# Kernel tuning notes

Hardware: AMD Instinct MI355X
Metric: run time of the kernel (lower is better)

Reference implementation:

```python
import jax, jax.numpy as jnp
import numpy as np

C = 0.01          # curvature
SQRT_C = C ** 0.5 # 0.1
R = 16            # number of diagonal blocks = out_features / block_size
BS = 256          # block_size
D = R * BS        # 4096


def _artanh(x):
    # Matches torch Artanh: clamp input, grad is 1/(1-xc^2) (straight-through clamp)
    xc = jnp.clip(x, -1.0 + 1e-5, 1.0 - 1e-5)
    xc = x + jax.lax.stop_gradient(xc - x)
    return 0.5 * (jnp.log(1.0 + xc) - jnp.log(1.0 - xc))


def _tanh(x, clamp=15.0):
    return jnp.tanh(jnp.clip(x, -clamp, clamp))


def _norm(x):
    return jnp.linalg.norm(x, axis=-1, keepdims=True)


def _forward(x, weights):
    # expmap0 (poincare ball)
    u_norm = jnp.maximum(_norm(x), 1e-5)
    h = _tanh(SQRT_C * u_norm) * x / (SQRT_C * u_norm)
    # fix_filt = output_hyperbolic.data  -> detach
    h = jax.lax.stop_gradient(h)

    # mobius_matvec with block-diagonal weight; equivalent batched block matmul:
    # mx = h @ block_diag(W_1..W_r).T  ==  per-block h_r @ W_r.T
    xb = h.reshape(h.shape[:-1] + (R, BS))            # [..., r, bs]
    mx = jnp.einsum('...rk,rjk->...rj', xb, weights)  # [..., r, bs]
    mx = mx.reshape(h.shape)

    x_norm = jnp.maximum(_norm(h), 1e-5)
    mx_norm = _norm(mx)
    res_c = _tanh(mx_norm / x_norm * _artanh(SQRT_C * x_norm)) * mx / (mx_norm * SQRT_C)
    cond = jnp.all(mx == 0, axis=-1, keepdims=True)
    res = jnp.where(cond, jnp.zeros((), dtype=res_c.dtype), res_c)

    # _project onto the ball
    nrm = jnp.maximum(_norm(res), 1e-5)
    maxnorm = (1.0 - 1e-3) / SQRT_C
    res = jnp.where(nrm > maxnorm, res / nrm * maxnorm, res)

    # logmap0 (poincare ball)
    y_norm = jnp.maximum(_norm(res), 1e-5)
    return res / y_norm / SQRT_C * _artanh(SQRT_C * y_norm)


def setup_inputs() -> dict:
    key = jax.random.key(0)
    k1, k2 = jax.random.split(key)
    x = jax.random.normal(k1, (4, 2048, D), dtype=jnp.float32)
    # params: init is stack of identity blocks; add small noise so math is non-trivial
    eye = jnp.broadcast_to(jnp.eye(BS, dtype=jnp.float32), (R, BS, BS))
    weights = eye + 0.02 * jax.random.normal(k2, (R, BS, BS), dtype=jnp.float32)
    return {"x": x, "weights": weights}


def reference(x, weights):
    return _forward(x, weights)
```

## Files before the change

kernel.cpp:

```cpp
#include <hip/hip_runtime.h>
#include <hip/hip_fp16.h>


typedef __attribute__((ext_vector_type(8))) short short8;
typedef __attribute__((ext_vector_type(4))) float f32x4;
typedef __attribute__((ext_vector_type(16))) float f32x16;

__device__ __forceinline__ ushort f2bf(float f) {
  uint u = __float_as_uint(f);
  return (ushort)((u + 0x7fffu + ((u >> 16) & 1u)) >> 16);
}

__device__ __forceinline__ float gamma_of(float sx, float s2) {
  const float xnorm = sqrtf(sx);
  const float un = fmaxf(xnorm, 1e-5f);
  const float a0 = 0.1f * un;
  const float th = tanhf(fminf(a0, 15.f));
  const float c = th / a0;
  const float hn = th * (xnorm / a0);
  const float xn = fmaxf(hn, 1e-5f);
  const float sp = sqrtf(s2);
  float gt = 0.f;
  if (sp > 0.f) {
    const float s = c * sp;
    const float xc = fminf(0.1f * xn, 1.f - 1e-5f);
    const float at = 0.5f * logf((1.f + xc) / (1.f - xc));
    const float t = (s / xn) * at;
    const float tn = tanhf(fminf(t, 15.f));
    const float alpha = tn / (0.1f * s);
    const float rn = tn * 10.f;
    const float nrm = fmaxf(rn, 1e-5f);
    const float proj = (nrm > 9.99f) ? (9.99f / nrm) : 1.f;
    const float yn = fmaxf(rn * proj, 1e-5f);
    const float yc = fminf(0.1f * yn, 1.f - 1e-5f);
    const float at2 = 0.5f * logf((1.f + yc) / (1.f - yc));
    gt = c * alpha * proj * (at2 / (0.1f * yn));
  }
  return gt;
}

__global__ __launch_bounds__(256) void wrepack32(const float* __restrict__ w,
                                                 ushort* __restrict__ wb3) {
  int idx = blockIdx.x * 256 + threadIdx.x;
  int lane = idx & 63;
  int nt = (idx >> 6) & 7;
  int kf = (idx >> 9) & 15;
  int b = idx >> 13;
  int n = nt * 32 + (lane & 31);
  int k0 = kf * 16 + (lane >> 5) * 8;
  const float* src = w + ((size_t)b << 16) + (size_t)n * 256 + k0;
  float4 v0 = *reinterpret_cast<const float4*>(src);
  float4 v1 = *reinterpret_cast<const float4*>(src + 4);
  uint4 p;
  p.x = (uint)f2bf(v0.x) | ((uint)f2bf(v0.y) << 16);
  p.y = (uint)f2bf(v0.z) | ((uint)f2bf(v0.w) << 16);
  p.z = (uint)f2bf(v1.x) | ((uint)f2bf(v1.y) << 16);
  p.w = (uint)f2bf(v1.z) | ((uint)f2bf(v1.w) << 16);
  reinterpret_cast<uint4*>(wb3)[idx] = p;
}

__global__ __launch_bounds__(256, 2) void k1_kernel(const float* __restrict__ x,
                                                    const ushort* __restrict__ wb3,
                                                    float* __restrict__ ssxP,
                                                    float* __restrict__ sspP,
                                                    ushort* __restrict__ mxw) {
  const int tid = threadIdx.x;
  const int w = tid >> 6;
  const int l = tid & 63;
  const int lo = l & 31;
  const int hi = l >> 5;
  const int b = blockIdx.x & 15;
  const int rg = blockIdx.x >> 4;
  const ushort* bbase = wb3 + ((size_t)b << 16);

  short8 B0[16], B1[16];
#pragma unroll
  for (int kf = 0; kf < 16; ++kf) {
    B0[kf] = *reinterpret_cast<const short8*>(bbase + (size_t)(kf * 8 + w * 2 + 0) * 512 + l * 8);
    B1[kf] = *reinterpret_cast<const short8*>(bbase + (size_t)(kf * 8 + w * 2 + 1) * 512 + l * 8);
  }

  for (int t = 0; t < 8; ++t) {
    const int rt = rg * 8 + t;
    const float* abase = x + ((size_t)rt * 32 + lo) * 4096 + b * 256 + hi * 8;

    f32x16 a0, a1;
#pragma unroll
    for (int r = 0; r < 16; ++r) { a0[r] = 0.f; a1[r] = 0.f; }
    float ssl = 0.f;

#pragma unroll
    for (int bb4 = 0; bb4 < 4; ++bb4) {
      float4 va[8];
#pragma unroll
      for (int k4 = 0; k4 < 4; ++k4) {
        const int kf = bb4 * 4 + k4;
        va[k4 * 2 + 0] = *reinterpret_cast<const float4*>(abase + kf * 16);
        va[k4 * 2 + 1] = *reinterpret_cast<const float4*>(abase + kf * 16 + 4);
      }
      if (w == 0) {
#pragma unroll
        for (int i = 0; i < 8; ++i)
          ssl += va[i].x * va[i].x + va[i].y * va[i].y + va[i].z * va[i].z + va[i].w * va[i].w;
      }
#pragma unroll
      for (int k4 = 0; k4 < 4; ++k4) {
        const int kf = bb4 * 4 + k4;
        const float4 v0 = va[k4 * 2], v1 = va[k4 * 2 + 1];
        short8 af;
        af[0] = (short)f2bf(v0.x); af[1] = (short)f2bf(v0.y);
        af[2] = (short)f2bf(v0.z); af[3] = (short)f2bf(v0.w);
        af[4] = (short)f2bf(v1.x); af[5] = (short)f2bf(v1.y);
        af[6] = (short)f2bf(v1.z); af[7] = (short)f2bf(v1.w);
        a0 = __builtin_amdgcn_mfma_f32_32x32x16_bf16(af, B0[kf], a0, 0, 0, 0);
        a1 = __builtin_amdgcn_mfma_f32_32x32x16_bf16(af, B1[kf], a1, 0, 0, 0);
      }
    }

    if (w == 0) {
      ssl += __shfl_xor(ssl, 32, 64);
      if (hi == 0) ssxP[b * 8192 + rt * 32 + lo] = ssl;
    }

    {
      float s[16];
#pragma unroll
      for (int r = 0; r < 16; ++r) s[r] = a0[r] * a0[r] + a1[r] * a1[r];
#pragma unroll
      for (int m = 1; m < 32; m <<= 1)
#pragma unroll
        for (int r = 0; r < 16; ++r) s[r] += __shfl_xor(s[r], m, 64);
      if (lo == 0) {
#pragma unroll
        for (int r = 0; r < 16; ++r) {
          const int rr = (r & 3) + 8 * (r >> 2) + 4 * hi;
          sspP[(size_t)(b * 4 + w) * 8192 + rt * 32 + rr] = s[r];
        }
      }
    }

    {
      uint wds[16];
#pragma unroll
      for (int j = 0; j < 8; ++j) {
        __half2 h0 = __floats2half2_rn(a0[2 * j], a0[2 * j + 1]);
        __half2 h1 = __floats2half2_rn(a1[2 * j], a1[2 * j + 1]);
        wds[j] = *reinterpret_cast<uint*>(&h0);
        wds[8 + j] = *reinterpret_cast<uint*>(&h1);
      }
      ushort* dst = mxw + (size_t)((b * 256 + rt) * 4 + w) * 2048;
#pragma unroll
      for (int i = 0; i < 4; ++i) {
        uint4 p;
        p.x = wds[i * 4 + 0]; p.y = wds[i * 4 + 1];
        p.z = wds[i * 4 + 2]; p.w = wds[i * 4 + 3];
        *reinterpret_cast<uint4*>(dst + (size_t)(i * 64 + l) * 8) = p;
      }
    }
  }
}

__global__ __launch_bounds__(256) void gamma_kernel(const float* __restrict__ ssxP,
                                                    const float* __restrict__ sspP,
                                                    float* __restrict__ gam) {
  const int row = blockIdx.x * 256 + threadIdx.x;
  float sx = 0.f, s2 = 0.f;
#pragma unroll
  for (int bb = 0; bb < 16; ++bb) sx += ssxP[bb * 8192 + row];
#pragma unroll
  for (int p = 0; p < 64; ++p) s2 += sspP[(size_t)p * 8192 + row];
  gam[row] = gamma_of(sx, s2);
}

__global__ __launch_bounds__(256) void k3_kernel(const ushort* __restrict__ mxw,
                                                 const float* __restrict__ gam,
                                                 float* __restrict__ out) {
  const int wt = blockIdx.x * 4 + (threadIdx.x >> 6);
  const int l = threadIdx.x & 63;
  const int lo = l & 31;
  const int hi = l >> 5;
  const int w = wt & 3;
  const int rt = (wt >> 2) & 255;
  const int b = wt >> 10;
  const ushort* src = mxw + (size_t)wt * 2048;
  uint4 p[4];
#pragma unroll
  for (int i = 0; i < 4; ++i)
    p[i] = *reinterpret_cast<const uint4*>(src + (size_t)(i * 64 + l) * 8);
  const int colbase = b * 256 + w * 64 + lo;
  const int rowb = rt * 32 + 4 * hi;
  const uint* pw = reinterpret_cast<const uint*>(p);
#pragma unroll
  for (int j = 0; j < 8; ++j) {
    const int r0 = 2 * j, r1 = 2 * j + 1;
    const int R0 = rowb + (r0 & 3) + 8 * (r0 >> 2);
    const int R1 = rowb + (r1 & 3) + 8 * (r1 >> 2);
    uint w0 = pw[j];
    uint w1 = pw[8 + j];
    float2 f0 = __half22float2(*reinterpret_cast<__half2*>(&w0));
    float2 f1 = __half22float2(*reinterpret_cast<__half2*>(&w1));
    const float g0 = gam[R0], g1 = gam[R1];
    out[(size_t)R0 * 4096 + colbase] = f0.x * g0;
    out[(size_t)R1 * 4096 + colbase] = f0.y * g1;
    out[(size_t)R0 * 4096 + colbase + 32] = f1.x * g0;
    out[(size_t)R1 * 4096 + colbase + 32] = f1.y * g1;
  }
}

__global__ __launch_bounds__(256) void wrepack16(const float* __restrict__ w,
                                                 ushort* __restrict__ wb2) {
  int idx = blockIdx.x * blockDim.x + threadIdx.x;
  int lane = idx & 63;
  int nt = (idx >> 6) & 15;
  int kf = (idx >> 10) & 7;
  int blk = idx >> 13;
  int g = lane >> 4, q = lane & 15;
  const float* src = w + ((size_t)blk << 16) + (size_t)(nt * 16 + q) * 256 + kf * 32 + g * 8;
  float4 v0 = *reinterpret_cast<const float4*>(src);
  float4 v1 = *reinterpret_cast<const float4*>(src + 4);
  uint4 p;
  p.x = (uint)f2bf(v0.x) | ((uint)f2bf(v0.y) << 16);
  p.y = (uint)f2bf(v0.z) | ((uint)f2bf(v0.w) << 16);
  p.z = (uint)f2bf(v1.x) | ((uint)f2bf(v1.y) << 16);
  p.w = (uint)f2bf(v1.z) | ((uint)f2bf(v1.w) << 16);
  reinterpret_cast<uint4*>(wb2)[idx] = p;
}

__global__ __launch_bounds__(1024, 4) void hyp_fused(const float* __restrict__ x,
                                                     const ushort* __restrict__ wb2,
                                                     float* __restrict__ out) {
  __shared__ ushort xs[16 * 4096];
  __shared__ float ssxp[16];
  __shared__ float sspm[16][16];
  __shared__ float gamv[16];
  const int tid = threadIdx.x;
  const int w = tid >> 6;
  const int lane = tid & 63;
  const int g = lane >> 4, q = lane & 15;
  const size_t rowbase = (size_t)blockIdx.x * 16;
  {
    const float4* xr = reinterpret_cast<const float4*>(x + (rowbase + w) * 4096);
    char* xrow = reinterpret_cast<char*>(xs);
    const uint sw = (uint)(w & 7) << 4;
    float ss = 0.f;
#pragma unroll
    for (int chunk = 0; chunk < 16; ++chunk) {
      float4 v = xr[chunk * 64 + lane];
      ss += v.x * v.x + v.y * v.y + v.z * v.z + v.w * v.w;
      uint2 p;
      p.x = (uint)f2bf(v.x) | ((uint)f2bf(v.y) << 16);
      p.y = (uint)f2bf(v.z) | ((uint)f2bf(v.w) << 16);
      uint byte = ((uint)(w * 8192 + (chunk * 64 + lane) * 8)) ^ sw;
      *reinterpret_cast<uint2*>(xrow + byte) = p;
    }
#pragma unroll
    for (int m = 32; m; m >>= 1) ss += __shfl_xor(ss, m, 64);
    if (lane == 0) ssxp[w] = ss;
  }
  __syncthreads();
  f32x4 acc[16];
#pragma unroll
  for (int nt = 0; nt < 16; ++nt) acc[nt] = (f32x4){0.f, 0.f, 0.f, 0.f};
  for (int kf = 0; kf < 8; ++kf) {
    uint abyte = ((uint)(q * 8192 + w * 512 + kf * 64 + g * 16)) ^ ((uint)(q & 7) << 4);
    short8 afr = *reinterpret_cast<const short8*>(reinterpret_cast<const char*>(xs) + abyte);
    const ushort* bkf = wb2 + ((((size_t)w * 8 + kf) * 16) << 9) + (lane << 3);
#pragma unroll
    for (int nt = 0; nt < 16; ++nt) {
      short8 bfr = *reinterpret_cast<const short8*>(bkf + (nt << 9));
      acc[nt] = __builtin_amdgcn_mfma_f32_16x16x32_bf16(afr, bfr, acc[nt], 0, 0, 0);
    }
  }
  {
    float s0 = 0.f, s1 = 0.f, s2a = 0.f, s3 = 0.f;
#pragma unroll
    for (int nt = 0; nt < 16; ++nt) {
      f32x4 a = acc[nt];
      s0 += a[0] * a[0]; s1 += a[1] * a[1]; s2a += a[2] * a[2]; s3 += a[3] * a[3];
    }
#pragma unroll
    for (int m = 1; m < 16; m <<= 1) {
      s0 += __shfl_xor(s0, m, 64); s1 += __shfl_xor(s1, m, 64);
      s2a += __shfl_xor(s2a, m, 64); s3 += __shfl_xor(s3, m, 64);
    }
    if (q == 0) {
      sspm[w][g * 4 + 0] = s0; sspm[w][g * 4 + 1] = s1;
      sspm[w][g * 4 + 2] = s2a; sspm[w][g * 4 + 3] = s3;
    }
  }
  __syncthreads();
  if (tid < 16) {
    float s2 = 0.f;
#pragma unroll
    for (int ww = 0; ww < 16; ++ww) s2 += sspm[ww][tid];
    gamv[tid] = gamma_of(ssxp[tid], s2);
  }
  __syncthreads();
  float gr[4];
#pragma unroll
  for (int j = 0; j < 4; ++j) gr[j] = gamv[g * 4 + j];
  float* orow = out + rowbase * 4096 + w * 256;
#pragma unroll
  for (int nt = 0; nt < 16; ++nt) {
    const int col = nt * 16 + q;
    f32x4 a = acc[nt];
#pragma unroll
    for (int j = 0; j < 4; ++j) orow[(size_t)(g * 4 + j) * 4096 + col] = gr[j] * a[j];
  }
}

extern "C" void kernel_launch(void* const* d_in, const int* in_sizes, int n_in,
                              void* d_out, int out_size, void* d_ws, size_t ws_size,
                              hipStream_t stream) {
  const float* x = (const float*)d_in[0];
  const float* w = (const float*)d_in[1];
  float* out = (float*)d_out;

  const size_t WB = (size_t)2 << 20;
  const size_t SSX_OFF = WB;
  const size_t SSP_OFF = WB + ((size_t)512 << 10);
  const size_t MXW_OFF = SSP_OFF + ((size_t)2 << 20);
  const size_t NEED = MXW_OFF + (size_t)16 * 8192 * 256 * 2;

  if (ws_size >= NEED) {
    ushort* wb3 = (ushort*)d_ws;
    float* ssxP = (float*)((char*)d_ws + SSX_OFF);
    float* sspP = (float*)((char*)d_ws + SSP_OFF);
    float* gamv = (float*)d_ws;
    ushort* mxw = (ushort*)((char*)d_ws + MXW_OFF);
    wrepack32<<<512, 256, 0, stream>>>(w, wb3);
    k1_kernel<<<512, 256, 0, stream>>>(x, wb3, ssxP, sspP, mxw);
    gamma_kernel<<<32, 256, 0, stream>>>(ssxP, sspP, gamv);
    k3_kernel<<<4096, 256, 0, stream>>>(mxw, gamv, out);
  } else if (ws_size >= WB) {
    ushort* wb2 = (ushort*)d_ws;
    wrepack16<<<512, 256, 0, stream>>>(w, wb2);
    hyp_fused<<<512, 1024, 0, stream>>>(x, wb2, out);
  }
}
```

Before: 138.7 us.

## Fuse matmul, norm reduction and scaling into one cooperative grid-synced kernel

Replaces the three-kernel path (k1 writing fp16 mx to workspace, gamma kernel, k3 rescaling) with one cooperative kernel. It keeps mx results in registers, reduces per-row norms in LDS, uses a grid-wide sync to combine the cross-block partial sums, then writes the scaled output directly. The aim is to drop the round trip of the intermediate mx buffer through global memory and two kernel launches. It also stages x through double-buffered LDS with register prefetch. In exchange it needs all 512 blocks co-resident (gated by an occupancy check) and pays for a grid barrier. The old 16-row fused fallback path is removed.

```diff
diff --git a/kernel.cpp b/kernel.cpp
--- a/kernel.cpp
+++ b/kernel.cpp
@@ -1,9 +1,11 @@
 #include <hip/hip_runtime.h>
 #include <hip/hip_fp16.h>
+#include <hip/hip_cooperative_groups.h>
+
+namespace cg = cooperative_groups;
 
 
 typedef __attribute__((ext_vector_type(8))) short short8;
-typedef __attribute__((ext_vector_type(4))) float f32x4;
 typedef __attribute__((ext_vector_type(16))) float f32x16;
 
 __device__ __forceinline__ ushort f2bf(float f) {
@@ -59,6 +61,139 @@
   reinterpret_cast<uint4*>(wb3)[idx] = p;
 }
 
+__global__ __launch_bounds__(512, 2) void hyp_coop(const float* __restrict__ x,
+                                                   const ushort* __restrict__ wb3,
+                                                   float* __restrict__ ssxP,
+                                                   float* __restrict__ sspP,
+                                                   float* __restrict__ out) {
+  __shared__ __align__(16) ushort Abuf[2][32 * 256];
+  __shared__ float sspw[8][256];
+  __shared__ float gl[256];
+
+  const int tid = threadIdx.x;
+  const int w = tid >> 6;
+  const int l = tid & 63;
+  const int lo = l & 31;
+  const int hi = l >> 5;
+  const int b = blockIdx.x & 15;
+  const int rg = blockIdx.x >> 4;
+  const size_t row0 = (size_t)rg * 256;
+
+  short8 B[16];
+  const ushort* bbase = wb3 + ((size_t)b << 16);
+#pragma unroll
+  for (int kf = 0; kf < 16; ++kf)
+    B[kf] = *reinterpret_cast<const short8*>(bbase + (size_t)(kf * 8 + w) * 512 + l * 8);
+
+  const int srow = tid >> 4;
+  const int seg = tid & 15;
+  const float* xsb = x + (row0 + srow) * 4096 + b * 256 + seg * 16;
+
+  uint mx[8][8];
+  float4 va[4];
+#pragma unroll
+  for (int j = 0; j < 4; ++j) va[j] = *reinterpret_cast<const float4*>(xsb + j * 4);
+
+#pragma unroll
+  for (int t = 0; t < 8; ++t) {
+    char* A = reinterpret_cast<char*>(Abuf[t & 1]);
+
+    {
+      float ss = 0.f;
+#pragma unroll
+      for (int j = 0; j < 4; ++j) {
+        float4 v = va[j];
+        ss += v.x * v.x + v.y * v.y + v.z * v.z + v.w * v.w;
+        uint2 p;
+        p.x = (uint)f2bf(v.x) | ((uint)f2bf(v.y) << 16);
+        p.y = (uint)f2bf(v.z) | ((uint)f2bf(v.w) << 16);
+        uint byte = ((uint)(srow * 512 + seg * 32 + j * 8)) ^ ((uint)(srow & 7) << 4);
+        *reinterpret_cast<uint2*>(A + byte) = p;
+      }
+      ss += __shfl_xor(ss, 1, 64);
+      ss += __shfl_xor(ss, 2, 64);
+      ss += __shfl_xor(ss, 4, 64);
+      ss += __shfl_xor(ss, 8, 64);
+      if (seg == 0) ssxP[b * 8192 + row0 + t * 32 + srow] = ss;
+    }
+    __syncthreads();
+
+    if (t < 7) {
+      const float* nx = xsb + (size_t)(t + 1) * 32 * 4096;
+#pragma unroll
+      for (int j = 0; j < 4; ++j) va[j] = *reinterpret_cast<const float4*>(nx + j * 4);
+    }
+
+    f32x16 acc;
+#pragma unroll
+    for (int r = 0; r < 16; ++r) acc[r] = 0.f;
+#pragma unroll
+    for (int kf = 0; kf < 16; ++kf) {
+      uint ab = ((uint)(lo * 512 + kf * 32 + hi * 16)) ^ ((uint)(lo & 7) << 4);
+      short8 af = *reinterpret_cast<const short8*>(A + ab);
+      acc = __builtin_amdgcn_mfma_f32_32x32x16_bf16(af, B[kf], acc, 0, 0, 0);
+    }
+
+#pragma unroll
+    for (int j = 0; j < 8; ++j) {
+      __half2 h = __floats2half2_rn(acc[2 * j], acc[2 * j + 1]);
+      mx[t][j] = *reinterpret_cast<uint*>(&h);
+    }
+
+    {
+      float s[16];
+#pragma unroll
+      for (int r = 0; r < 16; ++r) s[r] = acc[r] * acc[r];
+#pragma unroll
+      for (int m = 1; m < 32; m <<= 1)
+#pragma unroll
+        for (int r = 0; r < 16; ++r) s[r] += __shfl_xor(s[r], m, 64);
+      if (lo == 0) {
+#pragma unroll
+        for (int r = 0; r < 16; ++r)
+          sspw[w][t * 32 + (r & 3) + 8 * (r >> 2) + 4 * hi] = s[r];
+      }
+    }
+    __syncthreads();
+  }
+
+  if (tid < 256) {
+    float sp = 0.f;
+#pragma unroll
+    for (int ww = 0; ww < 8; ++ww) sp += sspw[ww][tid];
+    sspP[b * 8192 + row0 + tid] = sp;
+  }
+
+  cg::this_grid().sync();
+
+  if (tid < 256) {
+    const size_t row = row0 + tid;
+    float sx = 0.f, s2 = 0.f;
+#pragma unroll
+    for (int bb = 0; bb < 16; ++bb) {
+      sx += ssxP[bb * 8192 + row];
+      s2 += sspP[bb * 8192 + row];
+    }
+    gl[tid] = gamma_of(sx, s2);
+  }
+  __syncthreads();
+
+  const int col = b * 256 + w * 32 + lo;
+#pragma unroll
+  for (int t = 0; t < 8; ++t) {
+#pragma unroll
+    for (int j = 0; j < 8; ++j) {
+      const int r0 = 2 * j, r1 = 2 * j + 1;
+      const int lr0 = t * 32 + (r0 & 3) + 8 * (r0 >> 2) + 4 * hi;
+      const int lr1 = t * 32 + (r1 & 3) + 8 * (r1 >> 2) + 4 * hi;
+      uint pv = mx[t][j];
+      float2 f = __half22float2(*reinterpret_cast<__half2*>(&pv));
+      out[(row0 + lr0) * 4096 + col] = f.x * gl[lr0];
+      out[(row0 + lr1) * 4096 + col] = f.y * gl[lr1];
+    }
+  }
+}
+
 __global__ __launch_bounds__(256, 2) void k1_kernel(const float* __restrict__ x,
                                                     const ushort* __restrict__ wb3,
                                                     float* __restrict__ ssxP,
@@ -72,23 +207,19 @@
   const int b = blockIdx.x & 15;
   const int rg = blockIdx.x >> 4;
   const ushort* bbase = wb3 + ((size_t)b << 16);
-
   short8 B0[16], B1[16];
 #pragma unroll
   for (int kf = 0; kf < 16; ++kf) {
     B0[kf] = *reinterpret_cast<const short8*>(bbase + (size_t)(kf * 8 + w * 2 + 0) * 512 + l * 8);
     B1[kf] = *reinterpret_cast<const short8*>(bbase + (size_t)(kf * 8 + w * 2 + 1) * 512 + l * 8);
   }
-
   for (int t = 0; t < 8; ++t) {
     const int rt = rg * 8 + t;
     const float* abase = x + ((size_t)rt * 32 + lo) * 4096 + b * 256 + hi * 8;
-
     f32x16 a0, a1;
 #pragma unroll
     for (int r = 0; r < 16; ++r) { a0[r] = 0.f; a1[r] = 0.f; }
     float ssl = 0.f;
-
 #pragma unroll
     for (int bb4 = 0; bb4 < 4; ++bb4) {
       float4 va[8];
@@ -116,12 +247,10 @@
         a1 = __builtin_amdgcn_mfma_f32_32x32x16_bf16(af, B1[kf], a1, 0, 0, 0);
       }
     }
-
     if (w == 0) {
       ssl += __shfl_xor(ssl, 32, 64);
       if (hi == 0) ssxP[b * 8192 + rt * 32 + lo] = ssl;
     }
-
     {
       float s[16];
 #pragma unroll
@@ -138,7 +267,6 @@
         }
       }
     }
-
     {
       uint wds[16];
 #pragma unroll
@@ -207,108 +335,6 @@
   }
 }
 
-__global__ __launch_bounds__(256) void wrepack16(const float* __restrict__ w,
-                                                 ushort* __restrict__ wb2) {
-  int idx = blockIdx.x * blockDim.x + threadIdx.x;
-  int lane = idx & 63;
-  int nt = (idx >> 6) & 15;
-  int kf = (idx >> 10) & 7;
-  int blk = idx >> 13;
-  int g = lane >> 4, q = lane & 15;
-  const float* src = w + ((size_t)blk << 16) + (size_t)(nt * 16 + q) * 256 + kf * 32 + g * 8;
-  float4 v0 = *reinterpret_cast<const float4*>(src);
-  float4 v1 = *reinterpret_cast<const float4*>(src + 4);
-  uint4 p;
-  p.x = (uint)f2bf(v0.x) | ((uint)f2bf(v0.y) << 16);
-  p.y = (uint)f2bf(v0.z) | ((uint)f2bf(v0.w) << 16);
-  p.z = (uint)f2bf(v1.x) | ((uint)f2bf(v1.y) << 16);
-  p.w = (uint)f2bf(v1.z) | ((uint)f2bf(v1.w) << 16);
-  reinterpret_cast<uint4*>(wb2)[idx] = p;
-}
-
-__global__ __launch_bounds__(1024, 4) void hyp_fused(const float* __restrict__ x,
-                                                     const ushort* __restrict__ wb2,
-                                                     float* __restrict__ out) {
-  __shared__ ushort xs[16 * 4096];
-  __shared__ float ssxp[16];
-  __shared__ float sspm[16][16];
-  __shared__ float gamv[16];
-  const int tid = threadIdx.x;
-  const int w = tid >> 6;
-  const int lane = tid & 63;
-  const int g = lane >> 4, q = lane & 15;
-  const size_t rowbase = (size_t)blockIdx.x * 16;
-  {
-    const float4* xr = reinterpret_cast<const float4*>(x + (rowbase + w) * 4096);
-    char* xrow = reinterpret_cast<char*>(xs);
-    const uint sw = (uint)(w & 7) << 4;
-    float ss = 0.f;
-#pragma unroll
-    for (int chunk = 0; chunk < 16; ++chunk) {
-      float4 v = xr[chunk * 64 + lane];
-      ss += v.x * v.x + v.y * v.y + v.z * v.z + v.w * v.w;
-      uint2 p;
-      p.x = (uint)f2bf(v.x) | ((uint)f2bf(v.y) << 16);
-      p.y = (uint)f2bf(v.z) | ((uint)f2bf(v.w) << 16);
-      uint byte = ((uint)(w * 8192 + (chunk * 64 + lane) * 8)) ^ sw;
-      *reinterpret_cast<uint2*>(xrow + byte) = p;
-    }
-#pragma unroll
-    for (int m = 32; m; m >>= 1) ss += __shfl_xor(ss, m, 64);
-    if (lane == 0) ssxp[w] = ss;
-  }
-  __syncthreads();
-  f32x4 acc[16];
-#pragma unroll
-  for (int nt = 0; nt < 16; ++nt) acc[nt] = (f32x4){0.f, 0.f, 0.f, 0.f};
-  for (int kf = 0; kf < 8; ++kf) {
-    uint abyte = ((uint)(q * 8192 + w * 512 + kf * 64 + g * 16)) ^ ((uint)(q & 7) << 4);
-    short8 afr = *reinterpret_cast<const short8*>(reinterpret_cast<const char*>(xs) + abyte);
-    const ushort* bkf = wb2 + ((((size_t)w * 8 + kf) * 16) << 9) + (lane << 3);
-#pragma unroll
-    for (int nt = 0; nt < 16; ++nt) {
-      short8 bfr = *reinterpret_cast<const short8*>(bkf + (nt << 9));
-      acc[nt] = __builtin_amdgcn_mfma_f32_16x16x32_bf16(afr, bfr, acc[nt], 0, 0, 0);
-    }
-  }
-  {
-    float s0 = 0.f, s1 = 0.f, s2a = 0.f, s3 = 0.f;
-#pragma unroll
-    for (int nt = 0; nt < 16; ++nt) {
-      f32x4 a = acc[nt];
-      s0 += a[0] * a[0]; s1 += a[1] * a[1]; s2a += a[2] * a[2]; s3 += a[3] * a[3];
-    }
-#pragma unroll
-    for (int m = 1; m < 16; m <<= 1) {
-      s0 += __shfl_xor(s0, m, 64); s1 += __shfl_xor(s1, m, 64);
-      s2a += __shfl_xor(s2a, m, 64); s3 += __shfl_xor(s3, m, 64);
-    }
-    if (q == 0) {
-      sspm[w][g * 4 + 0] = s0; sspm[w][g * 4 + 1] = s1;
-      sspm[w][g * 4 + 2] = s2a; sspm[w][g * 4 + 3] = s3;
-    }
-  }
-  __syncthreads();
-  if (tid < 16) {
-    float s2 = 0.f;
-#pragma unroll
-    for (int ww = 0; ww < 16; ++ww) s2 += sspm[ww][tid];
-    gamv[tid] = gamma_of(ssxp[tid], s2);
-  }
-  __syncthreads();
-  float gr[4];
-#pragma unroll
-  for (int j = 0; j < 4; ++j) gr[j] = gamv[g * 4 + j];
-  float* orow = out + rowbase * 4096 + w * 256;
-#pragma unroll
-  for (int nt = 0; nt < 16; ++nt) {
-    const int col = nt * 16 + q;
-    f32x4 a = acc[nt];
-#pragma unroll
-    for (int j = 0; j < 4; ++j) orow[(size_t)(g * 4 + j) * 4096 + col] = gr[j] * a[j];
-  }
-}
-
 extern "C" void kernel_launch(void* const* d_in, const int* in_sizes, int n_in,
                               void* d_out, int out_size, void* d_ws, size_t ws_size,
                               hipStream_t stream) {
@@ -320,21 +346,27 @@
   const size_t SSX_OFF = WB;
   const size_t SSP_OFF = WB + ((size_t)512 << 10);
   const size_t MXW_OFF = SSP_OFF + ((size_t)2 << 20);
-  const size_t NEED = MXW_OFF + (size_t)16 * 8192 * 256 * 2;
-
-  if (ws_size >= NEED) {
-    ushort* wb3 = (ushort*)d_ws;
-    float* ssxP = (float*)((char*)d_ws + SSX_OFF);
-    float* sspP = (float*)((char*)d_ws + SSP_OFF);
+  const size_t NEED_COOP = SSP_OFF + ((size_t)512 << 10);
+  const size_t NEED_FULL = MXW_OFF + (size_t)16 * 8192 * 256 * 2;
+
+  ushort* wb3 = (ushort*)d_ws;
+  float* ssxP = (float*)((char*)d_ws + SSX_OFF);
+  float* sspP = (float*)((char*)d_ws + SSP_OFF);
+
+  int nb = 0;
+  bool coop_ok = (hipOccupancyMaxActiveBlocksPerMultiprocessor(&nb, hyp_coop, 512, 0) ==
+                  hipSuccess) && nb >= 2;
+
+  if (coop_ok && ws_size >= NEED_COOP) {
+    wrepack32<<<512, 256, 0, stream>>>(w, wb3);
+    void* args[5] = {(void*)&x, (void*)&wb3, (void*)&ssxP, (void*)&sspP, (void*)&out};
+    hipLaunchCooperativeKernel(hyp_coop, dim3(512), dim3(512), args, 0, stream);
+  } else if (ws_size >= NEED_FULL) {
     float* gamv = (float*)d_ws;
     ushort* mxw = (ushort*)((char*)d_ws + MXW_OFF);
     wrepack32<<<512, 256, 0, stream>>>(w, wb3);
     k1_kernel<<<512, 256, 0, stream>>>(x, wb3, ssxP, sspP, mxw);
     gamma_kernel<<<32, 256, 0, stream>>>(ssxP, sspP, gamv);
     k3_kernel<<<4096, 256, 0, stream>>>(mxw, gamv, out);
-  } else if (ws_size >= WB) {
-    ushort* wb2 = (ushort*)d_ws;
-    wrepack16<<<512, 256, 0, stream>>>(w, wb2);
-    hyp_fused<<<512, 1024, 0, stream>>>(x, wb2, out);
-  }
-}
+  }
+}
```

Result: no change. 138.7 us (-0.0%).
